# Performance work log

Hardware: AMD Instinct MI355X
Metric: run time of the kernel (lower is better)

The kernel has to match this reference:

```python
import jax, jax.numpy as jnp
import numpy as np

LOG2 = 0.6931471805599453
GAMMA = 10.0
NUM_KERNELS = 301
N_LAYERS = 3


def ssp(v):
    # ShiftedSoftplus: softplus(x) - log(2)
    return jax.nn.softplus(v) - jnp.asarray(LOG2, v.dtype)


def setup_inputs() -> dict:
    key = jax.random.key(0)
    ks = jax.random.split(key, 20)
    N, F, K, L, V = 512, 128, NUM_KERNELS, N_LAYERS, 100
    s = 0.05
    return {
        "x": jax.random.randint(ks[0], (N,), 0, V),
        "r": jax.random.uniform(ks[1], (N, 3), dtype=jnp.float32) * 10.0,
        "emb": jax.random.normal(ks[2], (V, F), dtype=jnp.float32),
        "aw_W": jax.random.normal(ks[3], (L, F, F), dtype=jnp.float32) * s,
        "aw_b": jax.random.normal(ks[4], (L, F), dtype=jnp.float32) * s,
        "cf_W1": jax.random.normal(ks[5], (L, K, F), dtype=jnp.float32) * s,
        "cf_b1": jax.random.normal(ks[6], (L, F), dtype=jnp.float32) * s,
        "cf_W2": jax.random.normal(ks[7], (L, F, F), dtype=jnp.float32) * s,
        "cf_b2": jax.random.normal(ks[8], (L, F), dtype=jnp.float32) * s,
        "n_W1": jax.random.normal(ks[9], (L, F, F), dtype=jnp.float32) * s,
        "n_b1": jax.random.normal(ks[10], (L, F), dtype=jnp.float32) * s,
        "n_W2": jax.random.normal(ks[11], (L, F, F), dtype=jnp.float32) * s,
        "n_b2": jax.random.normal(ks[12], (L, F), dtype=jnp.float32) * s,
        "out_W1": jax.random.normal(ks[13], (F, 32), dtype=jnp.float32) * s,
        "out_b1": jax.random.normal(ks[14], (32,), dtype=jnp.float32) * s,
        "out_W2": jax.random.normal(ks[15], (32, 1), dtype=jnp.float32) * s,
        "out_b2": jax.random.normal(ks[16], (1,), dtype=jnp.float32) * s,
    }


def reference(x, r, emb, aw_W, aw_b, cf_W1, cf_b1, cf_W2, cf_b2,
              n_W1, n_b1, n_W2, n_b2, out_W1, out_b1, out_W2, out_b2):
    centers = jnp.linspace(0.0, 30.0, NUM_KERNELS, dtype=r.dtype)  # [K]
    # pairwise distances (torch.cdist, p=2) with safe sqrt at the diagonal
    diff = r[:, None, :] - r[None, :, :]                 # [N,N,3]
    d2 = jnp.sum(diff * diff, axis=-1)                   # [N,N]
    mask = d2 > 0
    d = jnp.where(mask, jnp.sqrt(jnp.where(mask, d2, 1.0)), 0.0)

    h = emb[x]                                           # [N,F]
    for l in range(N_LAYERS):
        o = h @ aw_W[l] + aw_b[l]                        # atom-wise linear
        # Gaussian RBF expansion: [N,N,K]
        e = jnp.exp(-GAMMA * jnp.square(d[..., None] - centers))
        # filter-generating MLP: [N,N,F]
        w = ssp(e @ cf_W1[l] + cf_b1[l])
        w = ssp(w @ cf_W2[l] + cf_b2[l])
        # continuous-filter conv: o[i,k] = sum_j x[j,k] * w[i,j,k]
        c = jnp.einsum('jk,ijk->ik', o, w)
        c = ssp(c @ n_W1[l] + n_b1[l]) @ n_W2[l] + n_b2[l]
        h = h + c
    out = ssp(h @ out_W1 + out_b1) @ out_W2 + out_b2     # [N,1]
    # AdaptiveAvgPool1d(1) on a 2D [N,1] tensor is identity over L=1
    return out.reshape(-1)
```

## Files before the change

### kernel.cpp

```cpp
#include <hip/hip_runtime.h>
#include <hip/hip_fp16.h>
#include <math.h>

#define N_ATOMS 512
#define F_DIM   128
#define K_RBF   301
#define NLAYER  3
#define GAMMA_C 10.0f
#define LOG2_C  0.6931471805599453f

#define TAB_H     0.01f
#define TAB_INVH  100.0f
#define TAB_ROWS  1768
#define RPB       8
#define NGROUPS   (TAB_ROWS / RPB)
#define NTASKS    (NGROUPS * NLAYER)
#define NBBLK2    ((NTASKS + 1) / 2)
#define ROW_BYTES 512

__device__ __forceinline__ float ssp(float x) {
    float ax = fabsf(x);
    return fmaxf(x, 0.0f) + log1pf(expf(-ax)) - LOG2_C;
}
__device__ __forceinline__ __half2 u2h2(unsigned u) {
    union { unsigned u; __half2 h; } c; c.u = u; return c.h;
}
__device__ __forceinline__ unsigned h22u(__half2 h) {
    union { unsigned u; __half2 h; } c; c.h = h; return c.u;
}

__global__ void __launch_bounds__(256)
prep_build(const int* __restrict__ x, const float* __restrict__ r,
           const float* __restrict__ emb,
           const float* __restrict__ aw_W, const float* __restrict__ aw_b,
           const float* __restrict__ cf_W1, const float* __restrict__ cf_b1,
           const float* __restrict__ cf_W2, const float* __restrict__ cf_b2,
           uint2* __restrict__ dpk, float* __restrict__ h,
           unsigned* __restrict__ opk, uint2* __restrict__ ptab) {
    __shared__ float hs[F_DIM];
    __shared__ float os[F_DIM];
    __shared__ float e_s[2][RPB + 1][34];
    __shared__ float w1_s[2][F_DIM][12];

    if (blockIdx.x < N_ATOMS) {
        int i = blockIdx.x;
        int t = threadIdx.x;
        float rx = r[i * 3 + 0], ry = r[i * 3 + 1], rz = r[i * 3 + 2];
        if (t < F_DIM) {
            float hv = emb[x[i] * F_DIM + t];
            h[i * F_DIM + t] = hv;
            hs[t] = hv;
        }
        for (int j = t; j < N_ATOMS; j += 256) {
            float dx = rx - r[j * 3 + 0];
            float dy = ry - r[j * 3 + 1];
            float dz = rz - r[j * 3 + 2];
            float d  = sqrtf(dx * dx + dy * dy + dz * dz);
            float xb = d * TAB_INVH;
            int   b  = ::min((int)xb, TAB_ROWS - 2);
            float fr = xb - (float)b;
            __half fh = __float2half(fr);
            dpk[i * N_ATOMS + j] = make_uint2((unsigned)b * ROW_BYTES,
                                              h22u(__halves2half2(fh, fh)));
        }
        __syncthreads();
        if (t < F_DIM) {
            float acc = aw_b[t];
            for (int g = 0; g < F_DIM; ++g) acc = fmaf(hs[g], aw_W[g * F_DIM + t], acc);
            os[t] = acc;
        }
        __syncthreads();
        if (t < F_DIM / 2)
            opk[i * 64 + t] = h22u(__halves2half2(__float2half(os[2 * t]),
                                                  __float2half(os[2 * t + 1])));
        return;
    }

    int u = threadIdx.x >> 7;
    int f = threadIdx.x & 127;
    int task = (blockIdx.x - N_ATOMS) * 2 + u;
    bool valid = task < NTASKS;
    task = valid ? task : NTASKS - 1;
    int l    = task / NGROUPS;
    int row0 = (task % NGROUPS) * RPB;

    float dlo = row0 * TAB_H;
    float dhi = (row0 + RPB) * TAB_H;
    int k0 = ::max(0, (int)ceilf((dlo - 1.45f) * 10.0f));
    int k1 = ::min(K_RBF - 1, (int)floorf((dhi + 1.45f) * 10.0f));
    int kw = k1 - k0 + 1;

    for (int idx = f; idx < (RPB + 1) * kw; idx += F_DIM) {
        int rr = idx / kw, kk = idx % kw;
        float dv = (row0 + rr) * TAB_H;
        float tt = dv - 0.1f * (float)(k0 + kk);
        e_s[u][rr][kk] = expf(-GAMMA_C * tt * tt);
    }
    __syncthreads();

    const float* W1 = cf_W1 + l * K_RBF * F_DIM;
    float b1v = cf_b1[l * F_DIM + f];
    float acc[RPB + 1];
#pragma unroll
    for (int rr = 0; rr <= RPB; ++rr) acc[rr] = b1v;
    for (int kk = 0; kk < kw; ++kk) {
        float w1v = W1[(k0 + kk) * F_DIM + f];
#pragma unroll
        for (int rr = 0; rr <= RPB; ++rr) acc[rr] = fmaf(e_s[u][rr][kk], w1v, acc[rr]);
    }
#pragma unroll
    for (int rr = 0; rr <= RPB; ++rr) w1_s[u][f][rr] = ssp(acc[rr]);
    __syncthreads();

    const float* W2 = cf_W2 + l * F_DIM * F_DIM;
    float b2v = cf_b2[l * F_DIM + f];
    float acc2[RPB + 1];
#pragma unroll
    for (int rr = 0; rr <= RPB; ++rr) acc2[rr] = b2v;
    for (int g = 0; g < F_DIM; ++g) {
        float w2v = W2[g * F_DIM + f];
        float4 wa = *(const float4*)&w1_s[u][g][0];
        float4 wb = *(const float4*)&w1_s[u][g][4];
        float  wc = w1_s[u][g][8];
        acc2[0] = fmaf(wa.x, w2v, acc2[0]);
        acc2[1] = fmaf(wa.y, w2v, acc2[1]);
        acc2[2] = fmaf(wa.z, w2v, acc2[2]);
        acc2[3] = fmaf(wa.w, w2v, acc2[3]);
        acc2[4] = fmaf(wb.x, w2v, acc2[4]);
        acc2[5] = fmaf(wb.y, w2v, acc2[5]);
        acc2[6] = fmaf(wb.z, w2v, acc2[6]);
        acc2[7] = fmaf(wb.w, w2v, acc2[7]);
        acc2[8] = fmaf(wc,   w2v, acc2[8]);
    }
    float o9[RPB + 1];
#pragma unroll
    for (int rr = 0; rr <= RPB; ++rr) o9[rr] = ssp(acc2[rr]);

    if (valid) {
        int p = f >> 1;
        bool odd = (f & 1);
#pragma unroll
        for (int rr = 0; rr < RPB; ++rr) {
            float t0 = o9[rr];
            float dt = o9[rr + 1] - o9[rr];
            float ot0 = __shfl_xor(t0, 1, 64);
            float odt = __shfl_xor(dt, 1, 64);
            if (!odd) {
                uint2 v = make_uint2(
                    h22u(__halves2half2(__float2half(t0), __float2half(ot0))),
                    h22u(__halves2half2(__float2half(dt), __float2half(odt))));
                ptab[((size_t)l * TAB_ROWS + row0 + rr) * 64 + p] = v;
            }
        }
    }
}

__global__ void __launch_bounds__(512, 4)
convnode_kernel(const uint2* __restrict__ dpk, const unsigned* __restrict__ opk_in,
                const uint2* __restrict__ ptab,
                const float* __restrict__ n_W1, const float* __restrict__ n_b1,
                const float* __restrict__ n_W2, const float* __restrict__ n_b2,
                float* __restrict__ h,
                const float* __restrict__ aw_W, const float* __restrict__ aw_b,
                unsigned* __restrict__ opk_out,
                const float* __restrict__ oW1, const float* __restrict__ ob1,
                const float* __restrict__ oW2, const float* __restrict__ ob2,
                float* __restrict__ out, int l) {
    int i  = blockIdx.x;
    int t  = threadIdx.x;
    int p2 = t & 31;
    int jc = t >> 5;

    __shared__ __align__(16) uint2 ds[N_ATOMS];
    __shared__ __align__(16) float redbuf[16 * 32 * 4];
    __shared__ __align__(16) float cs[F_DIM];
    __shared__ __align__(16) float t1s[F_DIM];
    __shared__ __align__(16) float hs[F_DIM];

    ds[t] = dpk[i * N_ATOMS + t];
    if (t < F_DIM) hs[t] = h[i * F_DIM + t];
    __syncthreads();

    const char*  T   = (const char*)(ptab + (size_t)l * TAB_ROWS * 64) + p2 * 16;
    const uint2* ob  = (const uint2*)opk_in + p2;

    float4 acc = make_float4(0.0f, 0.0f, 0.0f, 0.0f);
    int j0 = jc * 32;
#pragma unroll 4
    for (int jj = 0; jj < 32; ++jj) {
        int j = j0 + jj;
        uint2 e = ds[j];
        uint4 tv = *(const uint4*)(T + e.x);
        uint2 ohu = ob[j * 32];
        __half2 fr2 = u2h2(e.y);
        __half2 wa = __hfma2(fr2, u2h2(tv.y), u2h2(tv.x));
        __half2 wb = __hfma2(fr2, u2h2(tv.w), u2h2(tv.z));
        __half2 oa = u2h2(ohu.x);
        __half2 obh = u2h2(ohu.y);
        acc.x = fmaf(__half2float(__low2half(wa)),  __half2float(__low2half(oa)),  acc.x);
        acc.y = fmaf(__half2float(__high2half(wa)), __half2float(__high2half(oa)), acc.y);
        acc.z = fmaf(__half2float(__low2half(wb)),  __half2float(__low2half(obh)), acc.z);
        acc.w = fmaf(__half2float(__high2half(wb)), __half2float(__high2half(obh)), acc.w);
    }
    *(float4*)&redbuf[(jc * 32 + p2) * 4] = acc;
    __syncthreads();
    if (t < 32) {
        float4 s = *(const float4*)&redbuf[t * 4];
#pragma unroll
        for (int q = 1; q < 16; ++q) {
            float4 v = *(const float4*)&redbuf[(q * 32 + t) * 4];
            s.x += v.x; s.y += v.y; s.z += v.z; s.w += v.w;
        }
        *(float4*)&cs[4 * t] = s;
    }
    __syncthreads();

    {
        int q = t >> 7, f = t & 127;
        const float* W1 = n_W1 + l * F_DIM * F_DIM;
        float a = 0.0f;
        int g0 = q * 32;
        for (int g = 0; g < 32; ++g) a = fmaf(cs[g0 + g], W1[(g0 + g) * F_DIM + f], a);
        redbuf[q * F_DIM + f] = a;
    }
    __syncthreads();
    if (t < F_DIM) {
        float a = redbuf[t] + redbuf[F_DIM + t] + redbuf[2 * F_DIM + t]
                + redbuf[3 * F_DIM + t] + n_b1[l * F_DIM + t];
        t1s[t] = ssp(a);
    }
    __syncthreads();

    {
        int q = t >> 7, f = t & 127;
        const float* W2 = n_W2 + l * F_DIM * F_DIM;
        float a = 0.0f;
        int g0 = q * 32;
        for (int g = 0; g < 32; ++g) a = fmaf(t1s[g0 + g], W2[(g0 + g) * F_DIM + f], a);
        redbuf[q * F_DIM + f] = a;
    }
    __syncthreads();
    if (t < F_DIM) {
        float a2 = redbuf[t] + redbuf[F_DIM + t] + redbuf[2 * F_DIM + t]
                 + redbuf[3 * F_DIM + t] + n_b2[l * F_DIM + t];
        float hv = hs[t] + a2;
        h[i * F_DIM + t] = hv;
        hs[t] = hv;
    }
    __syncthreads();

    if (l < NLAYER - 1) {
        {
            int q = t >> 7, f = t & 127;
            const float* W = aw_W + (l + 1) * F_DIM * F_DIM;
            float a = 0.0f;
            int g0 = q * 32;
            for (int g = 0; g < 32; ++g) a = fmaf(hs[g0 + g], W[(g0 + g) * F_DIM + f], a);
            redbuf[q * F_DIM + f] = a;
        }
        __syncthreads();
        if (t < F_DIM) {
            t1s[t] = redbuf[t] + redbuf[F_DIM + t] + redbuf[2 * F_DIM + t]
                   + redbuf[3 * F_DIM + t] + aw_b[(l + 1) * F_DIM + t];
        }
        __syncthreads();
        if (t < F_DIM / 2)
            opk_out[i * 64 + t] = h22u(__halves2half2(__float2half(t1s[2 * t]),
                                                      __float2half(t1s[2 * t + 1])));
    } else {
        {
            int q = t >> 5, f = t & 31;
            float a = 0.0f;
            int g0 = q * 8;
            for (int g = 0; g < 8; ++g) a = fmaf(hs[g0 + g], oW1[(g0 + g) * 32 + f], a);
            redbuf[q * 32 + f] = a;
        }
        __syncthreads();
        float val = 0.0f;
        if (t < 32) {
            float a = ob1[t];
#pragma unroll
            for (int q = 0; q < 16; ++q) a += redbuf[q * 32 + t];
            val = ssp(a) * oW2[t];
        }
#pragma unroll
        for (int off = 16; off > 0; off >>= 1) val += __shfl_xor(val, off, 64);
        if (t == 0) out[i] = val + ob2[0];
    }
}

extern "C" void kernel_launch(void* const* d_in, const int* in_sizes, int n_in,
                              void* d_out, int out_size, void* d_ws, size_t ws_size,
                              hipStream_t stream) {
    const int*   x     = (const int*)  d_in[0];
    const float* r     = (const float*)d_in[1];
    const float* emb   = (const float*)d_in[2];
    const float* aw_W  = (const float*)d_in[3];
    const float* aw_b  = (const float*)d_in[4];
    const float* cf_W1 = (const float*)d_in[5];
    const float* cf_b1 = (const float*)d_in[6];
    const float* cf_W2 = (const float*)d_in[7];
    const float* cf_b2 = (const float*)d_in[8];
    const float* n_W1  = (const float*)d_in[9];
    const float* n_b1  = (const float*)d_in[10];
    const float* n_W2  = (const float*)d_in[11];
    const float* n_b2  = (const float*)d_in[12];
    const float* oW1   = (const float*)d_in[13];
    const float* ob1   = (const float*)d_in[14];
    const float* oW2   = (const float*)d_in[15];
    const float* ob2   = (const float*)d_in[16];
    float* out = (float*)d_out;

    char* ws = (char*)d_ws;
    uint2*    dpk  = (uint2*)ws;    ws += (size_t)N_ATOMS * N_ATOMS * 8;
    float*    h    = (float*)ws;    ws += (size_t)N_ATOMS * F_DIM * 4;
    unsigned* opkA = (unsigned*)ws; ws += (size_t)N_ATOMS * (F_DIM / 2) * 4;
    unsigned* opkB = (unsigned*)ws; ws += (size_t)N_ATOMS * (F_DIM / 2) * 4;
    uint2*    ptab = (uint2*)ws;

    prep_build<<<N_ATOMS + NBBLK2, 256, 0, stream>>>(
        x, r, emb, aw_W, aw_b, cf_W1, cf_b1, cf_W2, cf_b2, dpk, h, opkA, ptab);
    for (int l = 0; l < NLAYER; ++l) {
        unsigned* oin  = (l & 1) ? opkB : opkA;
        unsigned* oout = (l & 1) ? opkA : opkB;
        convnode_kernel<<<N_ATOMS, 512, 0, stream>>>(
            dpk, oin, ptab, n_W1, n_b1, n_W2, n_b2, h,
            aw_W, aw_b, oout, oW1, ob1, oW2, ob2, out, l);
    }
}
```

Baseline: 168.4 us.

## Fuse three per-layer conv kernels into one persistent kernel with grid barriers

```diff
diff --git a/kernel.cpp b/kernel.cpp
--- a/kernel.cpp
+++ b/kernel.cpp
@@ -35,22 +35,20 @@
            const float* __restrict__ aw_W, const float* __restrict__ aw_b,
            const float* __restrict__ cf_W1, const float* __restrict__ cf_b1,
            const float* __restrict__ cf_W2, const float* __restrict__ cf_b2,
-           uint2* __restrict__ dpk, float* __restrict__ h,
-           unsigned* __restrict__ opk, uint2* __restrict__ ptab) {
+           uint2* __restrict__ dpk, unsigned* __restrict__ opk,
+           uint2* __restrict__ ptab, unsigned* __restrict__ sync) {
     __shared__ float hs[F_DIM];
     __shared__ float os[F_DIM];
     __shared__ float e_s[2][RPB + 1][34];
     __shared__ float w1_s[2][F_DIM][12];
 
+    if (blockIdx.x == 0 && threadIdx.x < 8) sync[threadIdx.x] = 0u;
+
     if (blockIdx.x < N_ATOMS) {
         int i = blockIdx.x;
         int t = threadIdx.x;
         float rx = r[i * 3 + 0], ry = r[i * 3 + 1], rz = r[i * 3 + 2];
-        if (t < F_DIM) {
-            float hv = emb[x[i] * F_DIM + t];
-            h[i * F_DIM + t] = hv;
-            hs[t] = hv;
-        }
+        if (t < F_DIM) hs[t] = emb[x[i] * F_DIM + t];
         for (int j = t; j < N_ATOMS; j += 256) {
             float dx = rx - r[j * 3 + 0];
             float dy = ry - r[j * 3 + 1];
@@ -155,17 +153,27 @@
     }
 }
 
+__device__ __forceinline__ void grid_barrier(unsigned* cnt) {
+    __syncthreads();
+    if (threadIdx.x == 0) {
+        __hip_atomic_fetch_add(cnt, 1u, __ATOMIC_ACQ_REL, __HIP_MEMORY_SCOPE_AGENT);
+        while (__hip_atomic_load(cnt, __ATOMIC_ACQUIRE, __HIP_MEMORY_SCOPE_AGENT)
+               < (unsigned)N_ATOMS)
+            __builtin_amdgcn_s_sleep(2);
+    }
+    __syncthreads();
+}
+
 __global__ void __launch_bounds__(512, 4)
-convnode_kernel(const uint2* __restrict__ dpk, const unsigned* __restrict__ opk_in,
-                const uint2* __restrict__ ptab,
-                const float* __restrict__ n_W1, const float* __restrict__ n_b1,
-                const float* __restrict__ n_W2, const float* __restrict__ n_b2,
-                float* __restrict__ h,
-                const float* __restrict__ aw_W, const float* __restrict__ aw_b,
-                unsigned* __restrict__ opk_out,
-                const float* __restrict__ oW1, const float* __restrict__ ob1,
-                const float* __restrict__ oW2, const float* __restrict__ ob2,
-                float* __restrict__ out, int l) {
+convnode3(const uint2* __restrict__ dpk, const int* __restrict__ x,
+          const float* __restrict__ emb, const uint2* __restrict__ ptab,
+          const float* __restrict__ n_W1, const float* __restrict__ n_b1,
+          const float* __restrict__ n_W2, const float* __restrict__ n_b2,
+          const float* __restrict__ aw_W, const float* __restrict__ aw_b,
+          unsigned* __restrict__ opkA, unsigned* __restrict__ opkB,
+          const float* __restrict__ oW1, const float* __restrict__ ob1,
+          const float* __restrict__ oW2, const float* __restrict__ ob2,
+          float* __restrict__ out, unsigned* __restrict__ sync) {
     int i  = blockIdx.x;
     int t  = threadIdx.x;
     int p2 = t & 31;
@@ -178,114 +186,118 @@
     __shared__ __align__(16) float hs[F_DIM];
 
     ds[t] = dpk[i * N_ATOMS + t];
-    if (t < F_DIM) hs[t] = h[i * F_DIM + t];
-    __syncthreads();
-
-    const char*  T   = (const char*)(ptab + (size_t)l * TAB_ROWS * 64) + p2 * 16;
-    const uint2* ob  = (const uint2*)opk_in + p2;
-
-    float4 acc = make_float4(0.0f, 0.0f, 0.0f, 0.0f);
-    int j0 = jc * 32;
+    if (t < F_DIM) hs[t] = emb[x[i] * F_DIM + t];
+    __syncthreads();
+
+    for (int l = 0; l < NLAYER; ++l) {
+        const unsigned* opk_in = (l & 1) ? opkB : opkA;
+        unsigned*       opk_out = (l & 1) ? opkA : opkB;
+
+        const char*  T  = (const char*)(ptab + (size_t)l * TAB_ROWS * 64) + p2 * 16;
+        const uint2* ob = (const uint2*)opk_in + p2;
+
+        float4 acc = make_float4(0.0f, 0.0f, 0.0f, 0.0f);
+        int j0 = jc * 32;
 #pragma unroll 4
-    for (int jj = 0; jj < 32; ++jj) {
-        int j = j0 + jj;
-        uint2 e = ds[j];
-        uint4 tv = *(const uint4*)(T + e.x);
-        uint2 ohu = ob[j * 32];
-        __half2 fr2 = u2h2(e.y);
-        __half2 wa = __hfma2(fr2, u2h2(tv.y), u2h2(tv.x));
-        __half2 wb = __hfma2(fr2, u2h2(tv.w), u2h2(tv.z));
-        __half2 oa = u2h2(ohu.x);
-        __half2 obh = u2h2(ohu.y);
-        acc.x = fmaf(__half2float(__low2half(wa)),  __half2float(__low2half(oa)),  acc.x);
-        acc.y = fmaf(__half2float(__high2half(wa)), __half2float(__high2half(oa)), acc.y);
-        acc.z = fmaf(__half2float(__low2half(wb)),  __half2float(__low2half(obh)), acc.z);
-        acc.w = fmaf(__half2float(__high2half(wb)), __half2float(__high2half(obh)), acc.w);
-    }
-    *(float4*)&redbuf[(jc * 32 + p2) * 4] = acc;
-    __syncthreads();
-    if (t < 32) {
-        float4 s = *(const float4*)&redbuf[t * 4];
-#pragma unroll
-        for (int q = 1; q < 16; ++q) {
-            float4 v = *(const float4*)&redbuf[(q * 32 + t) * 4];
-            s.x += v.x; s.y += v.y; s.z += v.z; s.w += v.w;
-        }
-        *(float4*)&cs[4 * t] = s;
-    }
-    __syncthreads();
-
-    {
-        int q = t >> 7, f = t & 127;
-        const float* W1 = n_W1 + l * F_DIM * F_DIM;
-        float a = 0.0f;
-        int g0 = q * 32;
-        for (int g = 0; g < 32; ++g) a = fmaf(cs[g0 + g], W1[(g0 + g) * F_DIM + f], a);
-        redbuf[q * F_DIM + f] = a;
-    }
-    __syncthreads();
-    if (t < F_DIM) {
-        float a = redbuf[t] + redbuf[F_DIM + t] + redbuf[2 * F_DIM + t]
-                + redbuf[3 * F_DIM + t] + n_b1[l * F_DIM + t];
-        t1s[t] = ssp(a);
-    }
-    __syncthreads();
-
-    {
-        int q = t >> 7, f = t & 127;
-        const float* W2 = n_W2 + l * F_DIM * F_DIM;
-        float a = 0.0f;
-        int g0 = q * 32;
-        for (int g = 0; g < 32; ++g) a = fmaf(t1s[g0 + g], W2[(g0 + g) * F_DIM + f], a);
-        redbuf[q * F_DIM + f] = a;
-    }
-    __syncthreads();
-    if (t < F_DIM) {
-        float a2 = redbuf[t] + redbuf[F_DIM + t] + redbuf[2 * F_DIM + t]
-                 + redbuf[3 * F_DIM + t] + n_b2[l * F_DIM + t];
-        float hv = hs[t] + a2;
-        h[i * F_DIM + t] = hv;
-        hs[t] = hv;
-    }
-    __syncthreads();
-
-    if (l < NLAYER - 1) {
+        for (int jj = 0; jj < 32; ++jj) {
+            int j = j0 + jj;
+            uint2 e = ds[j];
+            uint4 tv = *(const uint4*)(T + e.x);
+            uint2 ohu = ob[j * 32];
+            __half2 fr2 = u2h2(e.y);
+            __half2 wa = __hfma2(fr2, u2h2(tv.y), u2h2(tv.x));
+            __half2 wb = __hfma2(fr2, u2h2(tv.w), u2h2(tv.z));
+            __half2 oa = u2h2(ohu.x);
+            __half2 obh = u2h2(ohu.y);
+            acc.x = fmaf(__half2float(__low2half(wa)),  __half2float(__low2half(oa)),  acc.x);
+            acc.y = fmaf(__half2float(__high2half(wa)), __half2float(__high2half(oa)), acc.y);
+            acc.z = fmaf(__half2float(__low2half(wb)),  __half2float(__low2half(obh)), acc.z);
+            acc.w = fmaf(__half2float(__high2half(wb)), __half2float(__high2half(obh)), acc.w);
+        }
+        *(float4*)&redbuf[(jc * 32 + p2) * 4] = acc;
+        __syncthreads();
+        if (t < 32) {
+            float4 s = *(const float4*)&redbuf[t * 4];
+#pragma unroll
+            for (int q = 1; q < 16; ++q) {
+                float4 v = *(const float4*)&redbuf[(q * 32 + t) * 4];
+                s.x += v.x; s.y += v.y; s.z += v.z; s.w += v.w;
+            }
+            *(float4*)&cs[4 * t] = s;
+        }
+        __syncthreads();
+
         {
             int q = t >> 7, f = t & 127;
-            const float* W = aw_W + (l + 1) * F_DIM * F_DIM;
+            const float* W1 = n_W1 + l * F_DIM * F_DIM;
             float a = 0.0f;
             int g0 = q * 32;
-            for (int g = 0; g < 32; ++g) a = fmaf(hs[g0 + g], W[(g0 + g) * F_DIM + f], a);
+            for (int g = 0; g < 32; ++g) a = fmaf(cs[g0 + g], W1[(g0 + g) * F_DIM + f], a);
             redbuf[q * F_DIM + f] = a;
         }
         __syncthreads();
         if (t < F_DIM) {
-            t1s[t] = redbuf[t] + redbuf[F_DIM + t] + redbuf[2 * F_DIM + t]
-                   + redbuf[3 * F_DIM + t] + aw_b[(l + 1) * F_DIM + t];
-        }
-        __syncthreads();
-        if (t < F_DIM / 2)
-            opk_out[i * 64 + t] = h22u(__halves2half2(__float2half(t1s[2 * t]),
-                                                      __float2half(t1s[2 * t + 1])));
-    } else {
+            float a = redbuf[t] + redbuf[F_DIM + t] + redbuf[2 * F_DIM + t]
+                    + redbuf[3 * F_DIM + t] + n_b1[l * F_DIM + t];
+            t1s[t] = ssp(a);
+        }
+        __syncthreads();
+
         {
-            int q = t >> 5, f = t & 31;
+            int q = t >> 7, f = t & 127;
+            const float* W2 = n_W2 + l * F_DIM * F_DIM;
             float a = 0.0f;
-            int g0 = q * 8;
-            for (int g = 0; g < 8; ++g) a = fmaf(hs[g0 + g], oW1[(g0 + g) * 32 + f], a);
-            redbuf[q * 32 + f] = a;
-        }
-        __syncthreads();
-        float val = 0.0f;
-        if (t < 32) {
-            float a = ob1[t];
-#pragma unroll
-            for (int q = 0; q < 16; ++q) a += redbuf[q * 32 + t];
-            val = ssp(a) * oW2[t];
-        }
-#pragma unroll
-        for (int off = 16; off > 0; off >>= 1) val += __shfl_xor(val, off, 64);
-        if (t == 0) out[i] = val + ob2[0];
+            int g0 = q * 32;
+            for (int g = 0; g < 32; ++g) a = fmaf(t1s[g0 + g], W2[(g0 + g) * F_DIM + f], a);
+            redbuf[q * F_DIM + f] = a;
+        }
+        __syncthreads();
+        if (t < F_DIM) {
+            float a2 = redbuf[t] + redbuf[F_DIM + t] + redbuf[2 * F_DIM + t]
+                     + redbuf[3 * F_DIM + t] + n_b2[l * F_DIM + t];
+            hs[t] = hs[t] + a2;
+        }
+        __syncthreads();
+
+        if (l < NLAYER - 1) {
+            {
+                int q = t >> 7, f = t & 127;
+                const float* W = aw_W + (l + 1) * F_DIM * F_DIM;
+                float a = 0.0f;
+                int g0 = q * 32;
+                for (int g = 0; g < 32; ++g) a = fmaf(hs[g0 + g], W[(g0 + g) * F_DIM + f], a);
+                redbuf[q * F_DIM + f] = a;
+            }
+            __syncthreads();
+            if (t < F_DIM) {
+                t1s[t] = redbuf[t] + redbuf[F_DIM + t] + redbuf[2 * F_DIM + t]
+                       + redbuf[3 * F_DIM + t] + aw_b[(l + 1) * F_DIM + t];
+            }
+            __syncthreads();
+            if (t < F_DIM / 2)
+                opk_out[i * 64 + t] = h22u(__halves2half2(__float2half(t1s[2 * t]),
+                                                          __float2half(t1s[2 * t + 1])));
+            grid_barrier(&sync[l]);
+        } else {
+            {
+                int q = t >> 5, f = t & 31;
+                float a = 0.0f;
+                int g0 = q * 8;
+                for (int g = 0; g < 8; ++g) a = fmaf(hs[g0 + g], oW1[(g0 + g) * 32 + f], a);
+                redbuf[q * 32 + f] = a;
+            }
+            __syncthreads();
+            float val = 0.0f;
+            if (t < 32) {
+                float a = ob1[t];
+#pragma unroll
+                for (int q = 0; q < 16; ++q) a += redbuf[q * 32 + t];
+                val = ssp(a) * oW2[t];
+            }
+#pragma unroll
+            for (int off = 16; off > 0; off >>= 1) val += __shfl_xor(val, off, 64);
+            if (t == 0) out[i] = val + ob2[0];
+        }
     }
 }
 
@@ -313,18 +325,14 @@
 
     char* ws = (char*)d_ws;
     uint2*    dpk  = (uint2*)ws;    ws += (size_t)N_ATOMS * N_ATOMS * 8;
-    float*    h    = (float*)ws;    ws += (size_t)N_ATOMS * F_DIM * 4;
     unsigned* opkA = (unsigned*)ws; ws += (size_t)N_ATOMS * (F_DIM / 2) * 4;
     unsigned* opkB = (unsigned*)ws; ws += (size_t)N_ATOMS * (F_DIM / 2) * 4;
-    uint2*    ptab = (uint2*)ws;
+    uint2*    ptab = (uint2*)ws;    ws += (size_t)NLAYER * TAB_ROWS * 64 * 8;
+    unsigned* sync = (unsigned*)ws;
 
     prep_build<<<N_ATOMS + NBBLK2, 256, 0, stream>>>(
-        x, r, emb, aw_W, aw_b, cf_W1, cf_b1, cf_W2, cf_b2, dpk, h, opkA, ptab);
-    for (int l = 0; l < NLAYER; ++l) {
-        unsigned* oin  = (l & 1) ? opkB : opkA;
-        unsigned* oout = (l & 1) ? opkA : opkB;
-        convnode_kernel<<<N_ATOMS, 512, 0, stream>>>(
-            dpk, oin, ptab, n_W1, n_b1, n_W2, n_b2, h,
-            aw_W, aw_b, oout, oW1, ob1, oW2, ob2, out, l);
-    }
-}
+        x, r, emb, aw_W, aw_b, cf_W1, cf_b1, cf_W2, cf_b2, dpk, opkA, ptab, sync);
+    convnode3<<<N_ATOMS, 512, 0, stream>>>(
+        dpk, x, emb, ptab, n_W1, n_b1, n_W2, n_b2, aw_W, aw_b,
+        opkA, opkB, oW1, ob1, oW2, ob2, out, sync);
+}
```

Result: slower. 278.2 us (+65.1%).

## Split fused conv/node kernel into j-split conv kernel and separate node MLP kernel

Applied to the files above, without the earlier changes.

```diff
diff --git a/kernel.cpp b/kernel.cpp
--- a/kernel.cpp
+++ b/kernel.cpp
@@ -17,6 +17,9 @@
 #define NTASKS    (NGROUPS * NLAYER)
 #define NBBLK2    ((NTASKS + 1) / 2)
 #define ROW_BYTES 512
+
+#define JSPLIT  4
+#define JPB     (N_ATOMS / JSPLIT)
 
 __device__ __forceinline__ float ssp(float x) {
     float ax = fabsf(x);
@@ -155,39 +158,29 @@
     }
 }
 
-__global__ void __launch_bounds__(512, 4)
-convnode_kernel(const uint2* __restrict__ dpk, const unsigned* __restrict__ opk_in,
-                const uint2* __restrict__ ptab,
-                const float* __restrict__ n_W1, const float* __restrict__ n_b1,
-                const float* __restrict__ n_W2, const float* __restrict__ n_b2,
-                float* __restrict__ h,
-                const float* __restrict__ aw_W, const float* __restrict__ aw_b,
-                unsigned* __restrict__ opk_out,
-                const float* __restrict__ oW1, const float* __restrict__ ob1,
-                const float* __restrict__ oW2, const float* __restrict__ ob2,
-                float* __restrict__ out, int l) {
-    int i  = blockIdx.x;
-    int t  = threadIdx.x;
+__global__ void __launch_bounds__(256, 8)
+conv_kernel(const uint2* __restrict__ dpk, const unsigned* __restrict__ opk_in,
+            const uint2* __restrict__ ptab, float* __restrict__ c_part, int l) {
+    int bid = blockIdx.x;
+    int i = bid >> 2;
+    int q = bid & 3;
+    int t = threadIdx.x;
     int p2 = t & 31;
     int jc = t >> 5;
 
-    __shared__ __align__(16) uint2 ds[N_ATOMS];
-    __shared__ __align__(16) float redbuf[16 * 32 * 4];
-    __shared__ __align__(16) float cs[F_DIM];
-    __shared__ __align__(16) float t1s[F_DIM];
-    __shared__ __align__(16) float hs[F_DIM];
-
-    ds[t] = dpk[i * N_ATOMS + t];
-    if (t < F_DIM) hs[t] = h[i * F_DIM + t];
-    __syncthreads();
-
-    const char*  T   = (const char*)(ptab + (size_t)l * TAB_ROWS * 64) + p2 * 16;
-    const uint2* ob  = (const uint2*)opk_in + p2;
+    __shared__ __align__(16) uint2 ds[JPB];
+    __shared__ __align__(16) float redbuf[8 * 32 * 4];
+
+    if (t < JPB) ds[t] = dpk[i * N_ATOMS + q * JPB + t];
+    __syncthreads();
+
+    const char*  T  = (const char*)(ptab + (size_t)l * TAB_ROWS * 64) + p2 * 16;
+    const uint2* ob = (const uint2*)opk_in + p2 + (size_t)(q * JPB) * 32;
 
     float4 acc = make_float4(0.0f, 0.0f, 0.0f, 0.0f);
-    int j0 = jc * 32;
+    int j0 = jc * 16;
 #pragma unroll 4
-    for (int jj = 0; jj < 32; ++jj) {
+    for (int jj = 0; jj < 16; ++jj) {
         int j = j0 + jj;
         uint2 e = ds[j];
         uint4 tv = *(const uint4*)(T + e.x);
@@ -207,11 +200,36 @@
     if (t < 32) {
         float4 s = *(const float4*)&redbuf[t * 4];
 #pragma unroll
-        for (int q = 1; q < 16; ++q) {
-            float4 v = *(const float4*)&redbuf[(q * 32 + t) * 4];
+        for (int qq = 1; qq < 8; ++qq) {
+            float4 v = *(const float4*)&redbuf[(qq * 32 + t) * 4];
             s.x += v.x; s.y += v.y; s.z += v.z; s.w += v.w;
         }
-        *(float4*)&cs[4 * t] = s;
+        *(float4*)&c_part[((size_t)(i * JSPLIT + q)) * F_DIM + 4 * t] = s;
+    }
+}
+
+__global__ void __launch_bounds__(256)
+node_kernel(const float* __restrict__ c_part,
+            const float* __restrict__ n_W1, const float* __restrict__ n_b1,
+            const float* __restrict__ n_W2, const float* __restrict__ n_b2,
+            float* __restrict__ h,
+            const float* __restrict__ aw_W, const float* __restrict__ aw_b,
+            unsigned* __restrict__ opk_out,
+            const float* __restrict__ oW1, const float* __restrict__ ob1,
+            const float* __restrict__ oW2, const float* __restrict__ ob2,
+            float* __restrict__ out, int l) {
+    int i = blockIdx.x;
+    int t = threadIdx.x;
+
+    __shared__ __align__(16) float cs[F_DIM];
+    __shared__ __align__(16) float t1s[F_DIM];
+    __shared__ __align__(16) float hs[F_DIM];
+    __shared__ __align__(16) float redbuf[2 * F_DIM];
+
+    if (t < F_DIM) {
+        const float* cp = c_part + (size_t)i * JSPLIT * F_DIM + t;
+        cs[t] = (cp[0] + cp[F_DIM]) + (cp[2 * F_DIM] + cp[3 * F_DIM]);
+        hs[t] = h[i * F_DIM + t];
     }
     __syncthreads();
 
@@ -219,33 +237,28 @@
         int q = t >> 7, f = t & 127;
         const float* W1 = n_W1 + l * F_DIM * F_DIM;
         float a = 0.0f;
-        int g0 = q * 32;
-        for (int g = 0; g < 32; ++g) a = fmaf(cs[g0 + g], W1[(g0 + g) * F_DIM + f], a);
+        int g0 = q * 64;
+        for (int g = 0; g < 64; ++g) a = fmaf(cs[g0 + g], W1[(g0 + g) * F_DIM + f], a);
         redbuf[q * F_DIM + f] = a;
     }
     __syncthreads();
-    if (t < F_DIM) {
-        float a = redbuf[t] + redbuf[F_DIM + t] + redbuf[2 * F_DIM + t]
-                + redbuf[3 * F_DIM + t] + n_b1[l * F_DIM + t];
-        t1s[t] = ssp(a);
-    }
+    if (t < F_DIM)
+        t1s[t] = ssp(redbuf[t] + redbuf[F_DIM + t] + n_b1[l * F_DIM + t]);
     __syncthreads();
 
     {
         int q = t >> 7, f = t & 127;
         const float* W2 = n_W2 + l * F_DIM * F_DIM;
         float a = 0.0f;
-        int g0 = q * 32;
-        for (int g = 0; g < 32; ++g) a = fmaf(t1s[g0 + g], W2[(g0 + g) * F_DIM + f], a);
+        int g0 = q * 64;
+        for (int g = 0; g < 64; ++g) a = fmaf(t1s[g0 + g], W2[(g0 + g) * F_DIM + f], a);
         redbuf[q * F_DIM + f] = a;
     }
     __syncthreads();
     if (t < F_DIM) {
-        float a2 = redbuf[t] + redbuf[F_DIM + t] + redbuf[2 * F_DIM + t]
-                 + redbuf[3 * F_DIM + t] + n_b2[l * F_DIM + t];
-        float hv = hs[t] + a2;
-        h[i * F_DIM + t] = hv;
+        float hv = hs[t] + redbuf[t] + redbuf[F_DIM + t] + n_b2[l * F_DIM + t];
         hs[t] = hv;
+        if (l < NLAYER - 1) h[i * F_DIM + t] = hv;
     }
     __syncthreads();
 
@@ -254,14 +267,13 @@
             int q = t >> 7, f = t & 127;
             const float* W = aw_W + (l + 1) * F_DIM * F_DIM;
             float a = 0.0f;
-            int g0 = q * 32;
-            for (int g = 0; g < 32; ++g) a = fmaf(hs[g0 + g], W[(g0 + g) * F_DIM + f], a);
+            int g0 = q * 64;
+            for (int g = 0; g < 64; ++g) a = fmaf(hs[g0 + g], W[(g0 + g) * F_DIM + f], a);
             redbuf[q * F_DIM + f] = a;
         }
         __syncthreads();
         if (t < F_DIM) {
-            t1s[t] = redbuf[t] + redbuf[F_DIM + t] + redbuf[2 * F_DIM + t]
-                   + redbuf[3 * F_DIM + t] + aw_b[(l + 1) * F_DIM + t];
+            t1s[t] = redbuf[t] + redbuf[F_DIM + t] + aw_b[(l + 1) * F_DIM + t];
         }
         __syncthreads();
         if (t < F_DIM / 2)
@@ -271,8 +283,8 @@
         {
             int q = t >> 5, f = t & 31;
             float a = 0.0f;
-            int g0 = q * 8;
-            for (int g = 0; g < 8; ++g) a = fmaf(hs[g0 + g], oW1[(g0 + g) * 32 + f], a);
+            int g0 = q * 16;
+            for (int g = 0; g < 16; ++g) a = fmaf(hs[g0 + g], oW1[(g0 + g) * 32 + f], a);
             redbuf[q * 32 + f] = a;
         }
         __syncthreads();
@@ -280,7 +292,7 @@
         if (t < 32) {
             float a = ob1[t];
 #pragma unroll
-            for (int q = 0; q < 16; ++q) a += redbuf[q * 32 + t];
+            for (int q = 0; q < 8; ++q) a += redbuf[q * 32 + t];
             val = ssp(a) * oW2[t];
         }
 #pragma unroll
@@ -312,19 +324,21 @@
     float* out = (float*)d_out;
 
     char* ws = (char*)d_ws;
-    uint2*    dpk  = (uint2*)ws;    ws += (size_t)N_ATOMS * N_ATOMS * 8;
-    float*    h    = (float*)ws;    ws += (size_t)N_ATOMS * F_DIM * 4;
-    unsigned* opkA = (unsigned*)ws; ws += (size_t)N_ATOMS * (F_DIM / 2) * 4;
-    unsigned* opkB = (unsigned*)ws; ws += (size_t)N_ATOMS * (F_DIM / 2) * 4;
-    uint2*    ptab = (uint2*)ws;
+    uint2*    dpk    = (uint2*)ws;    ws += (size_t)N_ATOMS * N_ATOMS * 8;
+    float*    h      = (float*)ws;    ws += (size_t)N_ATOMS * F_DIM * 4;
+    unsigned* opkA   = (unsigned*)ws; ws += (size_t)N_ATOMS * (F_DIM / 2) * 4;
+    unsigned* opkB   = (unsigned*)ws; ws += (size_t)N_ATOMS * (F_DIM / 2) * 4;
+    uint2*    ptab   = (uint2*)ws;    ws += (size_t)NLAYER * TAB_ROWS * 64 * 8;
+    float*    c_part = (float*)ws;
 
     prep_build<<<N_ATOMS + NBBLK2, 256, 0, stream>>>(
         x, r, emb, aw_W, aw_b, cf_W1, cf_b1, cf_W2, cf_b2, dpk, h, opkA, ptab);
     for (int l = 0; l < NLAYER; ++l) {
         unsigned* oin  = (l & 1) ? opkB : opkA;
         unsigned* oout = (l & 1) ? opkA : opkB;
-        convnode_kernel<<<N_ATOMS, 512, 0, stream>>>(
-            dpk, oin, ptab, n_W1, n_b1, n_W2, n_b2, h,
-            aw_W, aw_b, oout, oW1, ob1, oW2, ob2, out, l);
-    }
-}
+        conv_kernel<<<N_ATOMS * JSPLIT, 256, 0, stream>>>(dpk, oin, ptab, c_part, l);
+        node_kernel<<<N_ATOMS, 256, 0, stream>>>(
+            c_part, n_W1, n_b1, n_W2, n_b2, h, aw_W, aw_b, oout,
+            oW1, ob1, oW2, ob2, out, l);
+    }
+}
```

After: 157.0 us. -6.8%, faster.

## Double per-atom block width to 1024 threads and batch table gathers

Applied to the files above, without the earlier changes.

```diff
diff --git a/kernel.cpp b/kernel.cpp
--- a/kernel.cpp
+++ b/kernel.cpp
@@ -39,6 +39,7 @@
            unsigned* __restrict__ opk, uint2* __restrict__ ptab) {
     __shared__ float hs[F_DIM];
     __shared__ float os[F_DIM];
+    __shared__ float red2[2 * F_DIM];
     __shared__ float e_s[2][RPB + 1][34];
     __shared__ float w1_s[2][F_DIM][12];
 
@@ -64,11 +65,16 @@
                                               h22u(__halves2half2(fh, fh)));
         }
         __syncthreads();
-        if (t < F_DIM) {
-            float acc = aw_b[t];
-            for (int g = 0; g < F_DIM; ++g) acc = fmaf(hs[g], aw_W[g * F_DIM + t], acc);
-            os[t] = acc;
-        }
+        {
+            int q = t >> 7, f = t & 127;
+            float a = 0.0f;
+            int g0 = q * 64;
+            for (int g = 0; g < 64; ++g)
+                a = fmaf(hs[g0 + g], aw_W[(g0 + g) * F_DIM + f], a);
+            red2[q * F_DIM + f] = a;
+        }
+        __syncthreads();
+        if (t < F_DIM) os[t] = red2[t] + red2[F_DIM + t] + aw_b[t];
         __syncthreads();
         if (t < F_DIM / 2)
             opk[i * 64 + t] = h22u(__halves2half2(__float2half(os[2 * t]),
@@ -155,63 +161,77 @@
     }
 }
 
-__global__ void __launch_bounds__(512, 4)
-convnode_kernel(const uint2* __restrict__ dpk, const unsigned* __restrict__ opk_in,
-                const uint2* __restrict__ ptab,
-                const float* __restrict__ n_W1, const float* __restrict__ n_b1,
-                const float* __restrict__ n_W2, const float* __restrict__ n_b2,
-                float* __restrict__ h,
-                const float* __restrict__ aw_W, const float* __restrict__ aw_b,
-                unsigned* __restrict__ opk_out,
-                const float* __restrict__ oW1, const float* __restrict__ ob1,
-                const float* __restrict__ oW2, const float* __restrict__ ob2,
-                float* __restrict__ out, int l) {
+__global__ void __launch_bounds__(1024, 8)
+layer_kernel(const uint2* __restrict__ dpk, const unsigned* __restrict__ opk_in,
+             const uint2* __restrict__ ptab,
+             const float* __restrict__ n_W1, const float* __restrict__ n_b1,
+             const float* __restrict__ n_W2, const float* __restrict__ n_b2,
+             float* __restrict__ h,
+             const float* __restrict__ aw_W, const float* __restrict__ aw_b,
+             unsigned* __restrict__ opk_out,
+             const float* __restrict__ oW1, const float* __restrict__ ob1,
+             const float* __restrict__ oW2, const float* __restrict__ ob2,
+             float* __restrict__ out, int l) {
     int i  = blockIdx.x;
     int t  = threadIdx.x;
     int p2 = t & 31;
     int jc = t >> 5;
 
     __shared__ __align__(16) uint2 ds[N_ATOMS];
-    __shared__ __align__(16) float redbuf[16 * 32 * 4];
+    __shared__ __align__(16) float redbuf[32 * 32 * 4];
     __shared__ __align__(16) float cs[F_DIM];
     __shared__ __align__(16) float t1s[F_DIM];
     __shared__ __align__(16) float hs[F_DIM];
 
-    ds[t] = dpk[i * N_ATOMS + t];
-    if (t < F_DIM) hs[t] = h[i * F_DIM + t];
-    __syncthreads();
-
-    const char*  T   = (const char*)(ptab + (size_t)l * TAB_ROWS * 64) + p2 * 16;
-    const uint2* ob  = (const uint2*)opk_in + p2;
+    if (t < N_ATOMS) ds[t] = dpk[i * N_ATOMS + t];
+    if (t >= N_ATOMS && t < N_ATOMS + F_DIM) hs[t - N_ATOMS] = h[i * F_DIM + (t - N_ATOMS)];
+    __syncthreads();
+
+    const char*  T  = (const char*)(ptab + (size_t)l * TAB_ROWS * 64) + p2 * 16;
+    const uint2* ob = (const uint2*)opk_in + p2;
 
     float4 acc = make_float4(0.0f, 0.0f, 0.0f, 0.0f);
-    int j0 = jc * 32;
-#pragma unroll 4
-    for (int jj = 0; jj < 32; ++jj) {
-        int j = j0 + jj;
-        uint2 e = ds[j];
-        uint4 tv = *(const uint4*)(T + e.x);
-        uint2 ohu = ob[j * 32];
-        __half2 fr2 = u2h2(e.y);
-        __half2 wa = __hfma2(fr2, u2h2(tv.y), u2h2(tv.x));
-        __half2 wb = __hfma2(fr2, u2h2(tv.w), u2h2(tv.z));
-        __half2 oa = u2h2(ohu.x);
-        __half2 obh = u2h2(ohu.y);
-        acc.x = fmaf(__half2float(__low2half(wa)),  __half2float(__low2half(oa)),  acc.x);
-        acc.y = fmaf(__half2float(__high2half(wa)), __half2float(__high2half(oa)), acc.y);
-        acc.z = fmaf(__half2float(__low2half(wb)),  __half2float(__low2half(obh)), acc.z);
-        acc.w = fmaf(__half2float(__high2half(wb)), __half2float(__high2half(obh)), acc.w);
+    int j0 = jc * 16;
+#pragma unroll
+    for (int b = 0; b < 4; ++b) {
+        uint4 wA = *(const uint4*)&ds[j0 + b * 4];
+        uint4 wB = *(const uint4*)&ds[j0 + b * 4 + 2];
+        uint2 e0 = make_uint2(wA.x, wA.y), e1 = make_uint2(wA.z, wA.w);
+        uint2 e2 = make_uint2(wB.x, wB.y), e3 = make_uint2(wB.z, wB.w);
+        uint4 tv0 = *(const uint4*)(T + e0.x);
+        uint4 tv1 = *(const uint4*)(T + e1.x);
+        uint4 tv2 = *(const uint4*)(T + e2.x);
+        uint4 tv3 = *(const uint4*)(T + e3.x);
+        uint2 oh0 = ob[(j0 + b * 4 + 0) * 32];
+        uint2 oh1 = ob[(j0 + b * 4 + 1) * 32];
+        uint2 oh2 = ob[(j0 + b * 4 + 2) * 32];
+        uint2 oh3 = ob[(j0 + b * 4 + 3) * 32];
+#define CONV_STEP(ee, tv, oh)                                                   \
+        {                                                                       \
+            __half2 fr2 = u2h2((ee).y);                                         \
+            __half2 wa = __hfma2(fr2, u2h2((tv).y), u2h2((tv).x));              \
+            __half2 wb = __hfma2(fr2, u2h2((tv).w), u2h2((tv).z));              \
+            __half2 oa  = u2h2((oh).x);                                         \
+            __half2 obh = u2h2((oh).y);                                         \
+            acc.x = fmaf(__half2float(__low2half(wa)),  __half2float(__low2half(oa)),  acc.x); \
+            acc.y = fmaf(__half2float(__high2half(wa)), __half2float(__high2half(oa)), acc.y); \
+            acc.z = fmaf(__half2float(__low2half(wb)),  __half2float(__low2half(obh)), acc.z); \
+            acc.w = fmaf(__half2float(__high2half(wb)), __half2float(__high2half(obh)), acc.w); \
+        }
+        CONV_STEP(e0, tv0, oh0)
+        CONV_STEP(e1, tv1, oh1)
+        CONV_STEP(e2, tv2, oh2)
+        CONV_STEP(e3, tv3, oh3)
+#undef CONV_STEP
     }
     *(float4*)&redbuf[(jc * 32 + p2) * 4] = acc;
     __syncthreads();
-    if (t < 32) {
-        float4 s = *(const float4*)&redbuf[t * 4];
-#pragma unroll
-        for (int q = 1; q < 16; ++q) {
-            float4 v = *(const float4*)&redbuf[(q * 32 + t) * 4];
-            s.x += v.x; s.y += v.y; s.z += v.z; s.w += v.w;
-        }
-        *(float4*)&cs[4 * t] = s;
+    if (t < F_DIM) {
+        int pr = t >> 2, c = t & 3;
+        float s = 0.0f;
+#pragma unroll
+        for (int g = 0; g < 32; ++g) s += redbuf[(g * 32 + pr) * 4 + c];
+        cs[t] = s;
     }
     __syncthreads();
 
@@ -219,14 +239,15 @@
         int q = t >> 7, f = t & 127;
         const float* W1 = n_W1 + l * F_DIM * F_DIM;
         float a = 0.0f;
-        int g0 = q * 32;
-        for (int g = 0; g < 32; ++g) a = fmaf(cs[g0 + g], W1[(g0 + g) * F_DIM + f], a);
+        int g0 = q * 16;
+        for (int g = 0; g < 16; ++g) a = fmaf(cs[g0 + g], W1[(g0 + g) * F_DIM + f], a);
         redbuf[q * F_DIM + f] = a;
     }
     __syncthreads();
     if (t < F_DIM) {
-        float a = redbuf[t] + redbuf[F_DIM + t] + redbuf[2 * F_DIM + t]
-                + redbuf[3 * F_DIM + t] + n_b1[l * F_DIM + t];
+        float a = n_b1[l * F_DIM + t];
+#pragma unroll
+        for (int q = 0; q < 8; ++q) a += redbuf[q * F_DIM + t];
         t1s[t] = ssp(a);
     }
     __syncthreads();
@@ -235,17 +256,18 @@
         int q = t >> 7, f = t & 127;
         const float* W2 = n_W2 + l * F_DIM * F_DIM;
         float a = 0.0f;
-        int g0 = q * 32;
-        for (int g = 0; g < 32; ++g) a = fmaf(t1s[g0 + g], W2[(g0 + g) * F_DIM + f], a);
+        int g0 = q * 16;
+        for (int g = 0; g < 16; ++g) a = fmaf(t1s[g0 + g], W2[(g0 + g) * F_DIM + f], a);
         redbuf[q * F_DIM + f] = a;
     }
     __syncthreads();
     if (t < F_DIM) {
-        float a2 = redbuf[t] + redbuf[F_DIM + t] + redbuf[2 * F_DIM + t]
-                 + redbuf[3 * F_DIM + t] + n_b2[l * F_DIM + t];
-        float hv = hs[t] + a2;
-        h[i * F_DIM + t] = hv;
+        float a = n_b2[l * F_DIM + t];
+#pragma unroll
+        for (int q = 0; q < 8; ++q) a += redbuf[q * F_DIM + t];
+        float hv = hs[t] + a;
         hs[t] = hv;
+        if (l < NLAYER - 1) h[i * F_DIM + t] = hv;
     }
     __syncthreads();
 
@@ -254,14 +276,16 @@
             int q = t >> 7, f = t & 127;
             const float* W = aw_W + (l + 1) * F_DIM * F_DIM;
             float a = 0.0f;
-            int g0 = q * 32;
-            for (int g = 0; g < 32; ++g) a = fmaf(hs[g0 + g], W[(g0 + g) * F_DIM + f], a);
+            int g0 = q * 16;
+            for (int g = 0; g < 16; ++g) a = fmaf(hs[g0 + g], W[(g0 + g) * F_DIM + f], a);
             redbuf[q * F_DIM + f] = a;
         }
         __syncthreads();
         if (t < F_DIM) {
-            t1s[t] = redbuf[t] + redbuf[F_DIM + t] + redbuf[2 * F_DIM + t]
-                   + redbuf[3 * F_DIM + t] + aw_b[(l + 1) * F_DIM + t];
+            float a = aw_b[(l + 1) * F_DIM + t];
+#pragma unroll
+            for (int q = 0; q < 8; ++q) a += redbuf[q * F_DIM + t];
+            t1s[t] = a;
         }
         __syncthreads();
         if (t < F_DIM / 2)
@@ -271,8 +295,8 @@
         {
             int q = t >> 5, f = t & 31;
             float a = 0.0f;
-            int g0 = q * 8;
-            for (int g = 0; g < 8; ++g) a = fmaf(hs[g0 + g], oW1[(g0 + g) * 32 + f], a);
+            int g0 = q * 4;
+            for (int g = 0; g < 4; ++g) a = fmaf(hs[g0 + g], oW1[(g0 + g) * 32 + f], a);
             redbuf[q * 32 + f] = a;
         }
         __syncthreads();
@@ -280,7 +304,7 @@
         if (t < 32) {
             float a = ob1[t];
 #pragma unroll
-            for (int q = 0; q < 16; ++q) a += redbuf[q * 32 + t];
+            for (int q = 0; q < 32; ++q) a += redbuf[q * 32 + t];
             val = ssp(a) * oW2[t];
         }
 #pragma unroll
@@ -323,8 +347,8 @@
     for (int l = 0; l < NLAYER; ++l) {
         unsigned* oin  = (l & 1) ? opkB : opkA;
         unsigned* oout = (l & 1) ? opkA : opkB;
-        convnode_kernel<<<N_ATOMS, 512, 0, stream>>>(
-            dpk, oin, ptab, n_W1, n_b1, n_W2, n_b2, h,
-            aw_W, aw_b, oout, oW1, ob1, oW2, ob2, out, l);
-    }
-}
+        layer_kernel<<<N_ATOMS, 1024, 0, stream>>>(
+            dpk, oin, ptab, n_W1, n_b1, n_W2, n_b2, h, aw_W, aw_b, oout,
+            oW1, ob1, oW2, ob2, out, l);
+    }
+}
```

After: 163.8 us. -2.8%, faster.
